# Kernel tuning notes

Hardware: AMD Instinct MI355X
Metric: run time of the kernel (lower is better)

The kernel has to match this reference:

```python
import jax, jax.numpy as jnp
import numpy as np

N = 100000      # nodes
E = 1280000     # random edges (self-loops added in reference, as PyG GATConv does)
F_IN = 12
HID = 64
HEADS = 4
G = 64          # graphs in batch
EPS_BN = 1e-5


def setup_inputs() -> dict:
    key = jax.random.key(0)
    ks = jax.random.split(key, 32)
    nrm = lambda k, s: jax.random.normal(k, s, jnp.float32) * 0.1
    inp = {
        "x": jax.random.normal(ks[0], (N, F_IN), jnp.float32),
        "edge_index": jax.random.randint(ks[1], (2, E), 0, N),
        "batch": jnp.sort(jax.random.randint(ks[2], (N,), 0, G)),
        # GATConv layer 1: in 12 -> 4 heads x 16, concat -> 64
        "W1": nrm(ks[3], (F_IN, HID)), "as1": nrm(ks[4], (HEADS, HID // HEADS)),
        "ad1": nrm(ks[5], (HEADS, HID // HEADS)), "b1": jnp.zeros((HID,), jnp.float32),
        "g1": jnp.ones((HID,), jnp.float32), "be1": jnp.zeros((HID,), jnp.float32),
        "W2": nrm(ks[6], (HID, HID)), "as2": nrm(ks[7], (HEADS, HID // HEADS)),
        "ad2": nrm(ks[8], (HEADS, HID // HEADS)), "b2": jnp.zeros((HID,), jnp.float32),
        "g2": jnp.ones((HID,), jnp.float32), "be2": jnp.zeros((HID,), jnp.float32),
        # GATConv layer 3: 64 -> 1 head x 64, concat=False (mean over 1 head)
        "W3": nrm(ks[9], (HID, HID)), "as3": nrm(ks[10], (1, HID)),
        "ad3": nrm(ks[11], (1, HID)), "b3": jnp.zeros((HID,), jnp.float32),
        "g3": jnp.ones((HID,), jnp.float32), "be3": jnp.zeros((HID,), jnp.float32),
        # classifier 64 -> 32 -> 2
        "Wc1": nrm(ks[12], (HID, HID // 2)), "bc1": jnp.zeros((HID // 2,), jnp.float32),
        "Wc2": nrm(ks[13], (HID // 2, 2)), "bc2": jnp.zeros((2,), jnp.float32),
        # embedding head 64 -> 64
        "We": nrm(ks[14], (HID, HID)), "bee": jnp.zeros((HID,), jnp.float32),
    }
    return inp


def _gat_layer(x, src, dst, W, a_src, a_dst, b, heads, concat):
    n = x.shape[0]
    c = W.shape[1] // heads
    h = (x @ W).reshape(n, heads, c)                      # [N,H,C]
    al_s = jnp.einsum('nhc,hc->nh', h, a_src)             # source term
    al_d = jnp.einsum('nhc,hc->nh', h, a_dst)             # target term
    e = jax.nn.leaky_relu(al_s[src] + al_d[dst], 0.2)     # [E,H]
    # segment softmax over incoming edges of each target node
    m = jax.ops.segment_max(e, dst, num_segments=n)
    ex = jnp.exp(e - m[dst])
    s = jax.ops.segment_sum(ex, dst, num_segments=n)
    alpha = ex / (s[dst] + 1e-16)                          # [E,H]
    msg = h[src] * alpha[:, :, None]                       # [E,H,C]
    out = jax.ops.segment_sum(msg, dst, num_segments=n)    # [N,H,C]
    out = out.reshape(n, heads * c) if concat else out.mean(axis=1)
    return out + b


def _bn(x, g, be):
    mu = x.mean(axis=0)
    var = x.var(axis=0)
    return (x - mu) * jax.lax.rsqrt(var + EPS_BN) * g + be


def reference(x, edge_index, batch,
              W1, as1, ad1, b1, g1, be1,
              W2, as2, ad2, b2, g2, be2,
              W3, as3, ad3, b3, g3, be3,
              Wc1, bc1, Wc2, bc2, We, bee):
    n = x.shape[0]
    loops = jnp.arange(n)
    src = jnp.concatenate([edge_index[0], loops])   # add self-loops (PyG default)
    dst = jnp.concatenate([edge_index[1], loops])

    h = _gat_layer(x, src, dst, W1, as1, ad1, b1, HEADS, True)
    h = jax.nn.elu(_bn(h, g1, be1))
    h = _gat_layer(h, src, dst, W2, as2, ad2, b2, HEADS, True)
    h = jax.nn.elu(_bn(h, g2, be2))
    h = _gat_layer(h, src, dst, W3, as3, ad3, b3, 1, False)
    h = jax.nn.elu(_bn(h, g3, be3))
    node_embeddings = h

    # global mean pool per graph
    sums = jax.ops.segment_sum(h, batch, num_segments=G)
    cnts = jax.ops.segment_sum(jnp.ones((n, 1), h.dtype), batch, num_segments=G)
    graph_emb = sums / jnp.maximum(cnts, 1.0)

    logits = jax.nn.relu(graph_emb @ Wc1 + bc1) @ Wc2 + bc2
    embedding = graph_emb @ We + bee
    return (logits, embedding, node_embeddings)
```

## Files before the change

### kernel.cpp

```cpp
#include <hip/hip_runtime.h>
#include <hip/hip_bf16.h>
#include <math.h>

#define THREADS 256
#define NBUCK 64
#define EPB 4096
#define RSB_SHIFT 8

__device__ __forceinline__ float lrelu02(float x) { return x >= 0.f ? x : 0.2f * x; }
__device__ __forceinline__ float b2f(__hip_bfloat16 v) { return __bfloat162float(v); }
__device__ __forceinline__ short f2bf_bits(float v) {
  __hip_bfloat16 hb = __float2bfloat16(v);
  return *reinterpret_cast<short*>(&hb);
}

using bf16x8 = __attribute__((ext_vector_type(8))) short;
using f32x4  = __attribute__((ext_vector_type(4))) float;

__global__ void count_tf1_k(const int* __restrict__ dstv, int* __restrict__ gcnt,
                            int E, int NBLK, int nbkt,
                            const float* __restrict__ x, const float* __restrict__ W1,
                            const float* __restrict__ aS, const float* __restrict__ aD,
                            __hip_bfloat16* __restrict__ h, float* __restrict__ als,
                            float* __restrict__ ald, int N, int nbNode,
                            const float* __restrict__ W2, const float* __restrict__ W3,
                            __hip_bfloat16* __restrict__ wt2, __hip_bfloat16* __restrict__ wt3,
                            int* __restrict__ offs, float* __restrict__ statsRep,
                            float* __restrict__ poolbuf, float* __restrict__ padA,
                            float* __restrict__ padB) {
  __shared__ int cnt[512];
  __shared__ float xs[4][12];
  int tid = threadIdx.x;
  if ((int)blockIdx.x < NBLK) {
    for (int i = tid; i < nbkt; i += THREADS) cnt[i] = 0;
    __syncthreads();
    int e0 = blockIdx.x * EPB;
    int e1 = e0 + EPB; if (e1 > E) e1 = E;
    for (int i = e0 + tid; i < e1; i += THREADS)
      atomicAdd(&cnt[__builtin_nontemporal_load(dstv + i) >> RSB_SHIFT], 1);
    __syncthreads();
    for (int i = tid; i < nbkt; i += THREADS)
      gcnt[(long long)i * NBLK + blockIdx.x] = cnt[i];
    return;
  }
  if ((int)blockIdx.x < NBLK + nbNode) {
    int wave = tid >> 6, lane = tid & 63;
    int n = (blockIdx.x - NBLK) * 4 + wave;
    if (n < N && lane < 12) xs[wave][lane] = x[(long long)n * 12 + lane];
    __syncthreads();
    if (n >= N) return;
    float acc = 0.f;
#pragma unroll
    for (int k = 0; k < 12; k++) acc += xs[wave][k] * W1[k * 64 + lane];
    h[(long long)n * 64 + lane] = __float2bfloat16(acc);
    float ts = acc * aS[lane], td = acc * aD[lane];
    for (int m = 1; m < 16; m <<= 1) {
      ts += __shfl_xor(ts, m, 64);
      td += __shfl_xor(td, m, 64);
    }
    if ((lane & 15) == 0) {
      int hh = lane >> 4;
      als[(long long)n * 4 + hh] = ts;
      ald[(long long)n * 4 + hh] = td;
    }
    return;
  }
  int pb = blockIdx.x - NBLK - nbNode;
  int gtid = pb * THREADS + tid;
  int stride = 32 * THREADS;
  if (gtid == 0) offs[N] = E;
  for (int i = gtid; i < 3 * NBUCK * 128; i += stride) statsRep[i] = 0.f;
  for (int i = gtid; i < 4096; i += stride) {
    poolbuf[i] = 0.f;
    padA[i] = 0.f;
    padB[i] = 0.f;
    int n = i >> 6, k = i & 63;
    wt2[n * 64 + k] = __float2bfloat16(W2[k * 64 + n]);
    wt3[n * 64 + k] = __float2bfloat16(W3[k * 64 + n]);
  }
}

__global__ void scan1_k(const int* __restrict__ in, int* __restrict__ out,
                        int* __restrict__ bsums, int L) {
  __shared__ int s[THREADS];
  int i = blockIdx.x * THREADS + threadIdx.x;
  int v = (i < L) ? in[i] : 0;
  s[threadIdx.x] = v;
  __syncthreads();
  for (int off = 1; off < THREADS; off <<= 1) {
    int t = (threadIdx.x >= off) ? s[threadIdx.x - off] : 0;
    __syncthreads();
    s[threadIdx.x] += t;
    __syncthreads();
  }
  if (i < L) out[i] = s[threadIdx.x] - v;
  if (threadIdx.x == THREADS - 1) bsums[blockIdx.x] = s[THREADS - 1];
}

__global__ void scan2_k(int* bsums, int nb) {
  __shared__ int s[1024];
  int tid = threadIdx.x;
  int v = (tid < nb) ? bsums[tid] : 0;
  s[tid] = v;
  __syncthreads();
  for (int off = 1; off < 1024; off <<= 1) {
    int t = (tid >= off) ? s[tid - off] : 0;
    __syncthreads();
    s[tid] += t;
    __syncthreads();
  }
  if (tid < nb) bsums[tid] = s[tid] - v;
}

__global__ void scan3b_k(int* __restrict__ a, const int* __restrict__ bsums, int L) {
  int i = blockIdx.x * THREADS + threadIdx.x;
  if (i < L) a[i] += bsums[blockIdx.x];
}

__global__ void binscatter_k(const int* __restrict__ srcv, const int* __restrict__ dstv,
                             const int* __restrict__ gbase, unsigned int* __restrict__ binned,
                             int E, int NBLK, int nbkt) {
  __shared__ int cur[512];
  int tid = threadIdx.x;
  int blk = blockIdx.x;
  for (int i = tid; i < nbkt; i += THREADS) cur[i] = gbase[(long long)i * NBLK + blk];
  __syncthreads();
  int e0 = blk * EPB;
  int e1 = e0 + EPB; if (e1 > E) e1 = E;
  for (int i = e0 + tid; i < e1; i += THREADS) {
    int d = __builtin_nontemporal_load(dstv + i);
    int s = __builtin_nontemporal_load(srcv + i);
    int p = atomicAdd(&cur[d >> RSB_SHIFT], 1);
    binned[p] = ((unsigned)s << 8) | (unsigned)(d & 255);
  }
}

__global__ void bucket_csr_k(const unsigned int* __restrict__ binned,
                             const int* __restrict__ gbase,
                             int* __restrict__ offs, int* __restrict__ csr,
                             int N, int E, int NBLK, int nbkt) {
  __shared__ int lcnt[256];
  __shared__ int lofs[256];
  int b = blockIdx.x;
  int lo = b << RSB_SHIFT;
  int tid = threadIdx.x;
  int b0 = gbase[(long long)b * NBLK];
  int b1 = (b + 1 < nbkt) ? gbase[(long long)(b + 1) * NBLK] : E;
  lcnt[tid] = 0;
  __syncthreads();
  for (int i = b0 + tid; i < b1; i += THREADS)
    atomicAdd(&lcnt[binned[i] & 255u], 1);
  __syncthreads();
  int v = lcnt[tid];
  lofs[tid] = v;
  __syncthreads();
  for (int off = 1; off < 256; off <<= 1) {
    int t = (tid >= off) ? lofs[tid - off] : 0;
    __syncthreads();
    lofs[tid] += t;
    __syncthreads();
  }
  int excl = lofs[tid] - v;
  int node = lo + tid;
  if (node < N) offs[node] = b0 + excl;
  lcnt[tid] = excl;
  __syncthreads();
  for (int i = b0 + tid; i < b1; i += THREADS) {
    unsigned e = binned[i];
    int r = atomicAdd(&lcnt[e & 255u], 1);
    csr[b0 + r] = (int)(e >> 8);
  }
}

__device__ __forceinline__ void compute_ssc(const float* __restrict__ rep,
                                            const float* __restrict__ g,
                                            const float* __restrict__ be,
                                            float* sscS, int N) {
  int tid = threadIdx.x;
  if (tid < 128) {
    float a = 0.f;
#pragma unroll 8
    for (int b = 0; b < NBUCK; b++) a += rep[b * 128 + tid];
    sscS[tid] = a;
  }
  __syncthreads();
  if (tid < 64) {
    float inv = 1.f / (float)N;
    float mu = sscS[tid] * inv;
    float var = sscS[64 + tid] * inv - mu * mu;
    float sc = rsqrtf(var + 1e-5f) * g[tid];
    sscS[tid] = sc;
    sscS[64 + tid] = be[tid] - mu * sc;
  }
  __syncthreads();
}

template <int H>
__global__ __launch_bounds__(256) void transform_mfma(
    const float* __restrict__ pre, const float* __restrict__ statsRep,
    const float* __restrict__ g0, const float* __restrict__ be0,
    const __hip_bfloat16* __restrict__ wt,
    const float* __restrict__ aS, const float* __restrict__ aD,
    __hip_bfloat16* __restrict__ h, float* __restrict__ als, float* __restrict__ ald,
    int N) {
  __shared__ float sscS[128];
  compute_ssc(statsRep, g0, be0, sscS, N);
  int wid = threadIdx.x >> 6, lane = threadIdx.x & 63;
  int m0 = blockIdx.x * 64 + wid * 16;
  int r = lane & 15, g = lane >> 4;
  const float* arow = pre + (long long)(m0 + r) * 64;
  int k0 = g * 8;
  bf16x8 a0, a1;
#pragma unroll
  for (int i = 0; i < 8; i++) {
    int ka = k0 + i, kb = k0 + 32 + i;
    float va = arow[ka] * sscS[ka] + sscS[64 + ka];
    float vb = arow[kb] * sscS[kb] + sscS[64 + kb];
    va = va > 0.f ? va : (__expf(va) - 1.f);
    vb = vb > 0.f ? vb : (__expf(vb) - 1.f);
    a0[i] = f2bf_bits(va);
    a1[i] = f2bf_bits(vb);
  }
  f32x4 acc[4];
#pragma unroll
  for (int s = 0; s < 4; s++) acc[s] = (f32x4){0.f, 0.f, 0.f, 0.f};
#pragma unroll
  for (int s = 0; s < 4; s++) {
    const bf16x8* brow = (const bf16x8*)(wt + (s * 16 + r) * 64 + k0);
    acc[s] = __builtin_amdgcn_mfma_f32_16x16x32_bf16(a0, brow[0], acc[s], 0, 0, 0);
    acc[s] = __builtin_amdgcn_mfma_f32_16x16x32_bf16(a1, brow[4], acc[s], 0, 0, 0);
  }
  float asum[4] = {0.f, 0.f, 0.f, 0.f}, dsum[4] = {0.f, 0.f, 0.f, 0.f};
#pragma unroll
  for (int s = 0; s < 4; s++) {
    int n = s * 16 + r;
    float sv = aS[n], dv = aD[n];
    float ts[4], td[4];
#pragma unroll
    for (int j = 0; j < 4; j++) { ts[j] = acc[s][j] * sv; td[j] = acc[s][j] * dv; }
#pragma unroll
    for (int mk = 1; mk < 16; mk <<= 1) {
#pragma unroll
      for (int j = 0; j < 4; j++) {
        ts[j] += __shfl_xor(ts[j], mk, 64);
        td[j] += __shfl_xor(td[j], mk, 64);
      }
    }
#pragma unroll
    for (int j = 0; j < 4; j++) {
      int m = m0 + g * 4 + j;
      if (m < N) {
        h[(long long)m * 64 + n] = __float2bfloat16(acc[s][j]);
        if (H == 4) {
          if (r == 0) { als[m * 4 + s] = ts[j]; ald[m * 4 + s] = td[j]; }
        }
      }
      if (H == 1) { asum[j] += ts[j]; dsum[j] += td[j]; }
    }
  }
  if (H == 1 && r == 0) {
#pragma unroll
    for (int j = 0; j < 4; j++) {
      int m = m0 + g * 4 + j;
      if (m < N) { als[m] = asum[j]; ald[m] = dsum[j]; }
    }
  }
}

__global__ void gat_gather4(const __hip_bfloat16* __restrict__ h, const float* __restrict__ als,
                            const float* __restrict__ ald, const int* __restrict__ offs,
                            const int* __restrict__ csr, const float* __restrict__ bias,
                            float* __restrict__ pre, float* __restrict__ statsRep, int N) {
  int wid = threadIdx.x >> 6, lane = threadIdx.x & 63;
  int n = blockIdx.x * 4 + wid;
  bool active = n < N;
  int t = lane & 3;
  int e = lane >> 2;
  int hh = lane >> 4;
  __shared__ float red[4][128];

  float v = 0.f;
  if (active) {
    float aldt = ald[n * 4 + t];
    float exs = __expf(lrelu02(als[n * 4 + t] + aldt));
    float sacc = 0.f;
    float acc = 0.f;
    int e0 = offs[n], e1 = offs[n + 1];

    for (int t0 = e0; t0 < e1; t0 += 16) {
      int idx = t0 + e;
      bool act = idx < e1;
      int sn = act ? csr[idx] : 0;
      float ex = act ? __expf(lrelu02(als[sn * 4 + t] + aldt)) : 0.f;
      sacc += ex;
#pragma unroll
      for (int j = 0; j < 16; j++) {
        int sj = __builtin_amdgcn_readlane(sn, j << 2);
        float exj = __shfl(ex, (j << 2) + hh, 64);
        acc += b2f(h[(long long)sj * 64 + lane]) * exj;
      }
    }
#pragma unroll
    for (int ms = 4; ms < 64; ms <<= 1) sacc += __shfl_xor(sacc, ms, 64);
    float s = sacc + exs;
    float exsb = __shfl(exs, hh, 64);
    float sb = __shfl(s, hh, 64);
    acc += b2f(h[(long long)n * 64 + lane]) * exsb;
    v = acc / (sb + 1e-16f) + bias[lane];
    pre[(long long)n * 64 + lane] = v;
  }
  red[wid][lane] = v;
  red[wid][64 + lane] = v * v;
  __syncthreads();
  if (threadIdx.x < 128) {
    float s4 = red[0][threadIdx.x] + red[1][threadIdx.x] + red[2][threadIdx.x] + red[3][threadIdx.x];
    atomicAdd(&statsRep[(blockIdx.x & (NBUCK - 1)) * 128 + threadIdx.x], s4);
  }
}

__global__ void gat_gather1(const __hip_bfloat16* __restrict__ h, const float* __restrict__ als,
                            const float* __restrict__ ald, const int* __restrict__ offs,
                            const int* __restrict__ csr, const float* __restrict__ bias,
                            float* __restrict__ pre, float* __restrict__ statsRep, int N) {
  int wid = threadIdx.x >> 6, lane = threadIdx.x & 63;
  int n = blockIdx.x * 4 + wid;
  bool active = n < N;
  __shared__ float red[4][128];

  float v = 0.f;
  if (active) {
    float aldn = ald[n];
    float exs = __expf(lrelu02(als[n] + aldn));
    float sacc = 0.f, acc = 0.f;
    int e0 = offs[n], e1 = offs[n + 1];

    for (int t0 = e0; t0 < e1; t0 += 64) {
      int idx = t0 + lane;
      bool act = idx < e1;
      int sn = act ? csr[idx] : 0;
      float ex = act ? __expf(lrelu02(als[sn] + aldn)) : 0.f;
      sacc += ex;
      int cnt = e1 - t0;
#pragma unroll
      for (int c = 0; c < 4; c++) {
        if (c * 16 >= cnt) break;
#pragma unroll
        for (int j = 0; j < 16; j++) {
          int ln = c * 16 + j;
          int sj = __builtin_amdgcn_readlane(sn, ln);
          float exj = __int_as_float(__builtin_amdgcn_readlane(__float_as_int(ex), ln));
          acc += b2f(h[(long long)sj * 64 + lane]) * exj;
        }
      }
    }
#pragma unroll
    for (int ms = 1; ms < 64; ms <<= 1) sacc += __shfl_xor(sacc, ms, 64);
    float s = sacc + exs;
    acc += b2f(h[(long long)n * 64 + lane]) * exs;
    v = acc / (s + 1e-16f) + bias[lane];
    pre[(long long)n * 64 + lane] = v;
  }
  red[wid][lane] = v;
  red[wid][64 + lane] = v * v;
  __syncthreads();
  if (threadIdx.x < 128) {
    float s4 = red[0][threadIdx.x] + red[1][threadIdx.x] + red[2][threadIdx.x] + red[3][threadIdx.x];
    atomicAdd(&statsRep[(blockIdx.x & (NBUCK - 1)) * 128 + threadIdx.x], s4);
  }
}

__global__ void emb_pool_k(const float* __restrict__ pre, const float* __restrict__ statsRep,
                           const float* __restrict__ g0, const float* __restrict__ be0,
                           const int* __restrict__ batch, float* __restrict__ nemb,
                           float* __restrict__ pool, int N, int per) {
  __shared__ float sscS[128];
  compute_ssc(statsRep, g0, be0, sscS, N);
  int lane = threadIdx.x & 63, wid = threadIdx.x >> 6;
  int gw = blockIdx.x * 4 + wid;
  int n0 = gw * per;
  int n1 = n0 + per; if (n1 > N) n1 = N;
  if (n0 >= n1) return;
  float sc = sscS[lane], sh = sscS[64 + lane];
  float acc = 0.f;
  int cg0 = batch[n0];
  for (int n = n0; n < n1; n++) {
    int g = batch[n];
    if (g != cg0) { atomicAdd(&pool[cg0 * 64 + lane], acc); acc = 0.f; cg0 = g; }
    float v = pre[(long long)n * 64 + lane] * sc + sh;
    v = v > 0.f ? v : (__expf(v) - 1.f);
    nemb[(long long)n * 64 + lane] = v;
    acc += v;
  }
  atomicAdd(&pool[cg0 * 64 + lane], acc);
}

__global__ void head_k(const float* __restrict__ pool, const int* __restrict__ batch,
                       const float* __restrict__ Wc1, const float* __restrict__ bc1,
                       const float* __restrict__ Wc2, const float* __restrict__ bc2,
                       const float* __restrict__ We, const float* __restrict__ bee,
                       float* __restrict__ logits, float* __restrict__ emb, int N) {
  int g = blockIdx.x, lane = threadIdx.x;
  __shared__ float pr[64], hid[32];
  __shared__ int bnds[2];
  if (lane < 2) {
    int target = g + lane;
    int lo = 0, hi = N;
    while (lo < hi) {
      int mid = (lo + hi) >> 1;
      if (batch[mid] < target) lo = mid + 1; else hi = mid;
    }
    bnds[lane] = lo;
  }
  __syncthreads();
  float cnt = (float)(bnds[1] - bnds[0]);
  pr[lane] = pool[g * 64 + lane] / fmaxf(cnt, 1.f);
  __syncthreads();
  if (lane < 32) {
    float a = bc1[lane];
    for (int k = 0; k < 64; k++) a += pr[k] * Wc1[k * 32 + lane];
    hid[lane] = fmaxf(a, 0.f);
  }
  float e = bee[lane];
  for (int k = 0; k < 64; k++) e += pr[k] * We[k * 64 + lane];
  emb[g * 64 + lane] = e;
  __syncthreads();
  if (lane < 2) {
    float l = bc2[lane];
    for (int k = 0; k < 32; k++) l += hid[k] * Wc2[k * 2 + lane];
    logits[g * 2 + lane] = l;
  }
}

extern "C" void kernel_launch(void* const* d_in, const int* in_sizes, int n_in,
                              void* d_out, int out_size, void* d_ws, size_t ws_size,
                              hipStream_t stream) {
  const float* x    = (const float*)d_in[0];
  const int*   ei   = (const int*)d_in[1];
  const int*   batch= (const int*)d_in[2];
  const float* W1   = (const float*)d_in[3];
  const float* as1  = (const float*)d_in[4];
  const float* ad1  = (const float*)d_in[5];
  const float* b1   = (const float*)d_in[6];
  const float* g1   = (const float*)d_in[7];
  const float* be1  = (const float*)d_in[8];
  const float* W2   = (const float*)d_in[9];
  const float* as2  = (const float*)d_in[10];
  const float* ad2  = (const float*)d_in[11];
  const float* b2   = (const float*)d_in[12];
  const float* g2   = (const float*)d_in[13];
  const float* be2  = (const float*)d_in[14];
  const float* W3   = (const float*)d_in[15];
  const float* as3  = (const float*)d_in[16];
  const float* ad3  = (const float*)d_in[17];
  const float* b3   = (const float*)d_in[18];
  const float* g3   = (const float*)d_in[19];
  const float* be3  = (const float*)d_in[20];
  const float* Wc1  = (const float*)d_in[21];
  const float* bc1  = (const float*)d_in[22];
  const float* Wc2  = (const float*)d_in[23];
  const float* bc2  = (const float*)d_in[24];
  const float* We   = (const float*)d_in[25];
  const float* bee  = (const float*)d_in[26];

  int N = in_sizes[0] / 12;
  int E = in_sizes[1] / 2;
  const int* srcv = ei;
  const int* dstv = ei + E;

  char* p = (char*)d_ws;
  auto carve = [&](size_t bytes) -> char* {
    char* r = p;
    p += (bytes + 255) & ~(size_t)255;
    return r;
  };
  int NBLK = (E + EPB - 1) / EPB;
  int nbkt = (N + 255) >> RSB_SHIFT;
  long long L = (long long)nbkt * NBLK;
  int Li = (int)L;
  int nbL = (Li + THREADS - 1) / THREADS;

  int* offs    = (int*)carve((size_t)(N + 1) * 4);
  int* gcnt    = (int*)carve((size_t)L * 4);
  int* gbase   = (int*)carve((size_t)L * 4);
  int* bsums   = (int*)carve(4096 * 4);
  int* csr     = (int*)carve((size_t)E * 4);
  unsigned int* binned = (unsigned int*)carve((size_t)E * 4);
  __hip_bfloat16* h  = (__hip_bfloat16*)carve((size_t)N * 64 * 2);
  __hip_bfloat16* wt2 = (__hip_bfloat16*)carve(64 * 64 * 2);
  __hip_bfloat16* wt3 = (__hip_bfloat16*)carve(64 * 64 * 2);
  float* als   = (float*)carve((size_t)N * 4 * 4);
  float* ald   = (float*)carve((size_t)N * 4 * 4);
  float* preA  = (float*)carve((size_t)(N + 64) * 64 * 4);
  float* preB  = (float*)carve((size_t)(N + 64) * 64 * 4);
  float* statsRep = (float*)carve(3 * NBUCK * 128 * 4);
  float* poolbuf  = (float*)carve(64 * 64 * 4);
  float* padA = preA + (size_t)N * 64;
  float* padB = preB + (size_t)N * 64;

  int nbNode = (N + 3) / 4;
  int nbT = (N + 63) / 64;

  count_tf1_k<<<NBLK + nbNode + 32, THREADS, 0, stream>>>(
      dstv, gcnt, E, NBLK, nbkt, x, W1, as1, ad1, h, als, ald, N, nbNode,
      W2, W3, wt2, wt3, offs, statsRep, poolbuf, padA, padB);
  scan1_k<<<nbL, THREADS, 0, stream>>>(gcnt, gbase, bsums, Li);
  scan2_k<<<1, 1024, 0, stream>>>(bsums, nbL);
  scan3b_k<<<nbL, THREADS, 0, stream>>>(gbase, bsums, Li);
  binscatter_k<<<NBLK, THREADS, 0, stream>>>(srcv, dstv, gbase, binned, E, NBLK, nbkt);
  bucket_csr_k<<<nbkt, THREADS, 0, stream>>>(binned, gbase, offs, csr, N, E, NBLK, nbkt);

  gat_gather4<<<nbNode, THREADS, 0, stream>>>(h, als, ald, offs, csr, b1, preA, statsRep, N);
  transform_mfma<4><<<nbT, THREADS, 0, stream>>>(preA, statsRep, g1, be1, wt2, as2, ad2, h, als, ald, N);
  gat_gather4<<<nbNode, THREADS, 0, stream>>>(h, als, ald, offs, csr, b2, preB, statsRep + NBUCK * 128, N);
  transform_mfma<1><<<nbT, THREADS, 0, stream>>>(preB, statsRep + NBUCK * 128, g2, be2, wt3, as3, ad3, h, als, ald, N);
  gat_gather1<<<nbNode, THREADS, 0, stream>>>(h, als, ald, offs, csr, b3, preA, statsRep + 2 * NBUCK * 128, N);

  float* outF   = (float*)d_out;
  float* logits = outF;
  float* emb    = outF + 64 * 2;
  float* nemb   = outF + 64 * 2 + 64 * 64;

  const int PER = 16;
  int nWaves = (N + PER - 1) / PER;
  int nbPool = (nWaves + 3) / 4;
  emb_pool_k<<<nbPool, THREADS, 0, stream>>>(preA, statsRep + 2 * NBUCK * 128, g3, be3,
                                             batch, nemb, poolbuf, N, PER);
  head_k<<<64, 64, 0, stream>>>(poolbuf, batch, Wc1, bc1, Wc2, bc2, We, bee, logits, emb, N);
}
```

Baseline: 292.7 us.

## Process several nodes per wave in gather kernels, merge scan passes, skip empty edge slots

The gather kernels now have each wave loop over 8 consecutive nodes instead of handling one. BN statistics are accumulated in registers across those nodes, so there are fewer blocks and fewer atomic stats writes. The inner neighbour loops are split into chunks of 4 that stop early when fewer edges remain, which avoids wasted gathers for low-degree tails. The second and third scan kernels are merged into one, where each block recomputes its prefix from the block sums, removing a launch at the cost of redundant reduction work. Fewer resident waves per node could reduce the latency hiding available for the random gathers.

Result: slower. 310.8 us (+6.2%).

```diff
diff --git a/kernel.cpp b/kernel.cpp
--- a/kernel.cpp
+++ b/kernel.cpp
@@ -6,6 +6,7 @@
 #define NBUCK 64
 #define EPB 4096
 #define RSB_SHIFT 8
+#define NPW 8
 
 __device__ __forceinline__ float lrelu02(float x) { return x >= 0.f ? x : 0.2f * x; }
 __device__ __forceinline__ float b2f(__hip_bfloat16 v) { return __bfloat162float(v); }
@@ -97,24 +98,20 @@
   if (threadIdx.x == THREADS - 1) bsums[blockIdx.x] = s[THREADS - 1];
 }
 
-__global__ void scan2_k(int* bsums, int nb) {
-  __shared__ int s[1024];
-  int tid = threadIdx.x;
-  int v = (tid < nb) ? bsums[tid] : 0;
-  s[tid] = v;
-  __syncthreads();
-  for (int off = 1; off < 1024; off <<= 1) {
-    int t = (tid >= off) ? s[tid - off] : 0;
-    __syncthreads();
-    s[tid] += t;
-    __syncthreads();
-  }
-  if (tid < nb) bsums[tid] = s[tid] - v;
-}
-
-__global__ void scan3b_k(int* __restrict__ a, const int* __restrict__ bsums, int L) {
-  int i = blockIdx.x * THREADS + threadIdx.x;
-  if (i < L) a[i] += bsums[blockIdx.x];
+__global__ void scan23_k(int* __restrict__ a, const int* __restrict__ bsums, int L) {
+  __shared__ int s[THREADS];
+  int tid = threadIdx.x, blk = blockIdx.x;
+  int acc = 0;
+  for (int i = tid; i < blk; i += THREADS) acc += bsums[i];
+  s[tid] = acc;
+  __syncthreads();
+  for (int off = 128; off > 0; off >>= 1) {
+    if (tid < off) s[tid] += s[tid + off];
+    __syncthreads();
+  }
+  int prefix = s[0];
+  int i = blk * THREADS + tid;
+  if (i < L) a[i] += prefix;
 }
 
 __global__ void binscatter_k(const int* __restrict__ srcv, const int* __restrict__ dstv,
@@ -272,15 +269,17 @@
                             const int* __restrict__ csr, const float* __restrict__ bias,
                             float* __restrict__ pre, float* __restrict__ statsRep, int N) {
   int wid = threadIdx.x >> 6, lane = threadIdx.x & 63;
-  int n = blockIdx.x * 4 + wid;
-  bool active = n < N;
   int t = lane & 3;
   int e = lane >> 2;
   int hh = lane >> 4;
   __shared__ float red[4][128];
-
-  float v = 0.f;
-  if (active) {
+  float bval = bias[lane];
+  float vs = 0.f, vq = 0.f;
+  int nbase = blockIdx.x * (4 * NPW) + wid * NPW;
+
+  for (int it = 0; it < NPW; it++) {
+    int n = nbase + it;
+    if (n >= N) break;
     float aldt = ald[n * 4 + t];
     float exs = __expf(lrelu02(als[n * 4 + t] + aldt));
     float sacc = 0.f;
@@ -293,11 +292,17 @@
       int sn = act ? csr[idx] : 0;
       float ex = act ? __expf(lrelu02(als[sn * 4 + t] + aldt)) : 0.f;
       sacc += ex;
-#pragma unroll
-      for (int j = 0; j < 16; j++) {
-        int sj = __builtin_amdgcn_readlane(sn, j << 2);
-        float exj = __shfl(ex, (j << 2) + hh, 64);
-        acc += b2f(h[(long long)sj * 64 + lane]) * exj;
+      int cnt = e1 - t0; if (cnt > 16) cnt = 16;
+#pragma unroll
+      for (int c = 0; c < 4; c++) {
+        if (c * 4 >= cnt) break;
+#pragma unroll
+        for (int jj = 0; jj < 4; jj++) {
+          int j = c * 4 + jj;
+          int sj = __builtin_amdgcn_readlane(sn, j << 2);
+          float exj = __shfl(ex, (j << 2) + hh, 64);
+          acc += b2f(h[(long long)sj * 64 + lane]) * exj;
+        }
       }
     }
 #pragma unroll
@@ -306,11 +311,13 @@
     float exsb = __shfl(exs, hh, 64);
     float sb = __shfl(s, hh, 64);
     acc += b2f(h[(long long)n * 64 + lane]) * exsb;
-    v = acc / (sb + 1e-16f) + bias[lane];
+    float v = acc / (sb + 1e-16f) + bval;
     pre[(long long)n * 64 + lane] = v;
-  }
-  red[wid][lane] = v;
-  red[wid][64 + lane] = v * v;
+    vs += v;
+    vq += v * v;
+  }
+  red[wid][lane] = vs;
+  red[wid][64 + lane] = vq;
   __syncthreads();
   if (threadIdx.x < 128) {
     float s4 = red[0][threadIdx.x] + red[1][threadIdx.x] + red[2][threadIdx.x] + red[3][threadIdx.x];
@@ -323,12 +330,14 @@
                             const int* __restrict__ csr, const float* __restrict__ bias,
                             float* __restrict__ pre, float* __restrict__ statsRep, int N) {
   int wid = threadIdx.x >> 6, lane = threadIdx.x & 63;
-  int n = blockIdx.x * 4 + wid;
-  bool active = n < N;
   __shared__ float red[4][128];
-
-  float v = 0.f;
-  if (active) {
+  float bval = bias[lane];
+  float vs = 0.f, vq = 0.f;
+  int nbase = blockIdx.x * (4 * NPW) + wid * NPW;
+
+  for (int it = 0; it < NPW; it++) {
+    int n = nbase + it;
+    if (n >= N) break;
     float aldn = ald[n];
     float exs = __expf(lrelu02(als[n] + aldn));
     float sacc = 0.f, acc = 0.f;
@@ -340,13 +349,13 @@
       int sn = act ? csr[idx] : 0;
       float ex = act ? __expf(lrelu02(als[sn] + aldn)) : 0.f;
       sacc += ex;
-      int cnt = e1 - t0;
-#pragma unroll
-      for (int c = 0; c < 4; c++) {
-        if (c * 16 >= cnt) break;
-#pragma unroll
-        for (int j = 0; j < 16; j++) {
-          int ln = c * 16 + j;
+      int cnt = e1 - t0; if (cnt > 64) cnt = 64;
+#pragma unroll
+      for (int c = 0; c < 16; c++) {
+        if (c * 4 >= cnt) break;
+#pragma unroll
+        for (int jj = 0; jj < 4; jj++) {
+          int ln = c * 4 + jj;
           int sj = __builtin_amdgcn_readlane(sn, ln);
           float exj = __int_as_float(__builtin_amdgcn_readlane(__float_as_int(ex), ln));
           acc += b2f(h[(long long)sj * 64 + lane]) * exj;
@@ -357,11 +366,13 @@
     for (int ms = 1; ms < 64; ms <<= 1) sacc += __shfl_xor(sacc, ms, 64);
     float s = sacc + exs;
     acc += b2f(h[(long long)n * 64 + lane]) * exs;
-    v = acc / (s + 1e-16f) + bias[lane];
+    float v = acc / (s + 1e-16f) + bval;
     pre[(long long)n * 64 + lane] = v;
-  }
-  red[wid][lane] = v;
-  red[wid][64 + lane] = v * v;
+    vs += v;
+    vq += v * v;
+  }
+  red[wid][lane] = vs;
+  red[wid][64 + lane] = vq;
   __syncthreads();
   if (threadIdx.x < 128) {
     float s4 = red[0][threadIdx.x] + red[1][threadIdx.x] + red[2][threadIdx.x] + red[3][threadIdx.x];
@@ -498,22 +509,22 @@
   float* padB = preB + (size_t)N * 64;
 
   int nbNode = (N + 3) / 4;
+  int nbG = (N + 4 * NPW - 1) / (4 * NPW);
   int nbT = (N + 63) / 64;
 
   count_tf1_k<<<NBLK + nbNode + 32, THREADS, 0, stream>>>(
       dstv, gcnt, E, NBLK, nbkt, x, W1, as1, ad1, h, als, ald, N, nbNode,
       W2, W3, wt2, wt3, offs, statsRep, poolbuf, padA, padB);
   scan1_k<<<nbL, THREADS, 0, stream>>>(gcnt, gbase, bsums, Li);
-  scan2_k<<<1, 1024, 0, stream>>>(bsums, nbL);
-  scan3b_k<<<nbL, THREADS, 0, stream>>>(gbase, bsums, Li);
+  scan23_k<<<nbL, THREADS, 0, stream>>>(gbase, bsums, Li);
   binscatter_k<<<NBLK, THREADS, 0, stream>>>(srcv, dstv, gbase, binned, E, NBLK, nbkt);
   bucket_csr_k<<<nbkt, THREADS, 0, stream>>>(binned, gbase, offs, csr, N, E, NBLK, nbkt);
 
-  gat_gather4<<<nbNode, THREADS, 0, stream>>>(h, als, ald, offs, csr, b1, preA, statsRep, N);
+  gat_gather4<<<nbG, THREADS, 0, stream>>>(h, als, ald, offs, csr, b1, preA, statsRep, N);
   transform_mfma<4><<<nbT, THREADS, 0, stream>>>(preA, statsRep, g1, be1, wt2, as2, ad2, h, als, ald, N);
-  gat_gather4<<<nbNode, THREADS, 0, stream>>>(h, als, ald, offs, csr, b2, preB, statsRep + NBUCK * 128, N);
+  gat_gather4<<<nbG, THREADS, 0, stream>>>(h, als, ald, offs, csr, b2, preB, statsRep + NBUCK * 128, N);
   transform_mfma<1><<<nbT, THREADS, 0, stream>>>(preB, statsRep + NBUCK * 128, g2, be2, wt3, as3, ad3, h, als, ald, N);
-  gat_gather1<<<nbNode, THREADS, 0, stream>>>(h, als, ald, offs, csr, b3, preA, statsRep + 2 * NBUCK * 128, N);
+  gat_gather1<<<nbG, THREADS, 0, stream>>>(h, als, ald, offs, csr, b3, preA, statsRep + 2 * NBUCK * 128, N);
 
   float* outF   = (float*)d_out;
   float* logits = outF;
```
